# Kernel tuning notes

Measured on AMD Instinct MI355X. Metric: run time of the kernel, lower is better.

Reference implementation:

```python
import jax, jax.numpy as jnp
import numpy as np

B, IN, OUT = 512, 1023, 512
CLIP = 2.0
LN_EPS = 1e-5


def setup_inputs() -> dict:
    key = jax.random.key(0)
    ks = jax.random.split(key, 10)
    x = jax.random.normal(ks[0], (B, IN), dtype=jnp.float32)
    hebb = jax.random.normal(ks[1], (B, IN + 1, OUT), dtype=jnp.float32)
    weight = 0.001 * jax.random.normal(ks[2], (IN + 1, OUT), dtype=jnp.float32)
    alpha = 0.001 * jax.random.normal(ks[3], (IN + 1, OUT), dtype=jnp.float32)
    ln_gamma = jnp.ones((OUT,), dtype=jnp.float32)
    ln_beta = jnp.zeros((OUT,), dtype=jnp.float32)
    # modulator: Linear(OUT, 1)
    mod_w = jax.random.uniform(ks[4], (1, OUT), dtype=jnp.float32,
                               minval=-1.0, maxval=1.0) / np.sqrt(OUT)
    mod_b = jax.random.uniform(ks[5], (1,), dtype=jnp.float32,
                               minval=-1.0, maxval=1.0) / np.sqrt(OUT)
    # modfanout: Linear(1, OUT)
    fan_w = jax.random.uniform(ks[6], (OUT, 1), dtype=jnp.float32,
                               minval=-1.0, maxval=1.0)
    fan_b = jax.random.uniform(ks[7], (OUT,), dtype=jnp.float32,
                               minval=-1.0, maxval=1.0)
    return {"x": x, "hebb": hebb, "weight": weight, "alpha": alpha,
            "ln_gamma": ln_gamma, "ln_beta": ln_beta,
            "mod_w": mod_w, "mod_b": mod_b, "fan_w": fan_w, "fan_b": fan_b}


def reference(x, hebb, weight, alpha, ln_gamma, ln_beta, mod_w, mod_b, fan_w, fan_b):
    # pad bias column of ones: [B, IN+1]
    xp = jnp.concatenate([x, jnp.ones((x.shape[0], 1), dtype=x.dtype)], axis=-1)
    # per-sample effective weights: [B, IN+1, OUT]
    w_eff = weight[None] + alpha[None] * hebb
    y_pre = jnp.einsum('bi,bio->bo', xp, w_eff)  # [B, OUT]
    # LayerNorm over last dim
    mu = jnp.mean(y_pre, axis=-1, keepdims=True)
    var = jnp.mean(jnp.square(y_pre - mu), axis=-1, keepdims=True)
    y = jnp.tanh(ln_gamma * (y_pre - mu) * jax.lax.rsqrt(var + LN_EPS) + ln_beta)
    # modulator scalar per sample: [B, 1]
    m = jnp.tanh(y @ mod_w.T + mod_b)
    # fanout eta: [B, 1, OUT]
    eta = m[:, :, None] * fan_w[:, 0][None, None, :] + fan_b[None, None, :]
    # outer-product Hebbian update: [B, IN+1, OUT]
    delta = eta * (xp[:, :, None] * y[:, None, :])
    hebb_new = jnp.clip(hebb + delta, -CLIP, CLIP)
    return (y, m, hebb_new)
```

## Files before the change

### kernel.cpp

```cpp
#include <hip/hip_runtime.h>
#include <cstddef>

#define B_       512
#define IN_      1023
#define INP1     1024
#define OUT_     512
#define OUT4     128
#define CLIPV    2.0f
#define LNEPS    1e-5f
#define SLABS    4
#define SLABROWS 256

typedef float fx4 __attribute__((ext_vector_type(4)));

__device__ __forceinline__ float2 block_reduce2(float a, float b, float2* lds) {
    #pragma unroll
    for (int off = 32; off; off >>= 1) {
        a += __shfl_down(a, off, 64);
        b += __shfl_down(b, off, 64);
    }
    const int lane = threadIdx.x & 63;
    const int wid  = threadIdx.x >> 6;
    const int nw   = blockDim.x >> 6;
    if (lane == 0) lds[wid] = make_float2(a, b);
    __syncthreads();
    if (wid == 0) {
        float2 v = (lane < nw) ? lds[lane] : make_float2(0.f, 0.f);
        a = v.x; b = v.y;
        #pragma unroll
        for (int off = 8; off; off >>= 1) {
            a += __shfl_down(a, off, 64);
            b += __shfl_down(b, off, 64);
        }
        if (lane == 0) lds[0] = make_float2(a, b);
    }
    __syncthreads();
    float2 r = lds[0];
    __syncthreads();
    return r;
}

__global__ __launch_bounds__(256) void k1a_partial(
    const float* __restrict__ x, const float* __restrict__ hebb,
    const float* __restrict__ weight, const float* __restrict__ alpha,
    float* __restrict__ ws_part)
{
    const int bs   = blockIdx.x;
    const int b    = bs >> 2;
    const int s    = bs & 3;
    const int tid  = threadIdx.x;
    const int o4   = tid & 127;
    const int half = tid >> 7;

    __shared__ float  xs[SLABROWS];
    __shared__ float4 part[2][OUT4];

    {
        const int i = s * SLABROWS + tid;
        xs[tid] = (i < IN_) ? x[(size_t)b * IN_ + i] : 1.0f;
    }
    __syncthreads();

    const int i0 = s * SLABROWS + half * 128;
    const float4* __restrict__ h4 = (const float4*)hebb  + ((size_t)b * INP1 + i0) * OUT4 + o4;
    const float4* __restrict__ w4 = (const float4*)weight + (size_t)i0 * OUT4 + o4;
    const float4* __restrict__ a4 = (const float4*)alpha  + (size_t)i0 * OUT4 + o4;
    const float* __restrict__ xk = xs + half * 128;

    float4 acc = make_float4(0.f, 0.f, 0.f, 0.f);
    #pragma unroll 4
    for (int k = 0; k < 128; ++k) {
        const float  xv = xk[k];
        const float4 h  = h4[(size_t)k * OUT4];
        const float4 w  = w4[(size_t)k * OUT4];
        const float4 a  = a4[(size_t)k * OUT4];
        acc.x = fmaf(xv, fmaf(a.x, h.x, w.x), acc.x);
        acc.y = fmaf(xv, fmaf(a.y, h.y, w.y), acc.y);
        acc.z = fmaf(xv, fmaf(a.z, h.z, w.z), acc.z);
        acc.w = fmaf(xv, fmaf(a.w, h.w, w.w), acc.w);
    }

    part[half][o4] = acc;
    __syncthreads();
    if (half == 0) {
        float4 p = part[0][o4];
        const float4 q = part[1][o4];
        p.x += q.x; p.y += q.y; p.z += q.z; p.w += q.w;
        ((float4*)ws_part)[(size_t)bs * OUT4 + o4] = p;
    }
}

__global__ __launch_bounds__(512) void k1b_ln_mod(
    const float* __restrict__ ws_part,
    const float* __restrict__ ln_g, const float* __restrict__ ln_b,
    const float* __restrict__ mod_w, const float* __restrict__ mod_b,
    float* __restrict__ y_out, float* __restrict__ m_out)
{
    const int b = blockIdx.x;
    const int o = threadIdx.x;
    __shared__ float2 rbuf[16];

    float ypre = 0.f;
    #pragma unroll
    for (int s = 0; s < SLABS; ++s)
        ypre += ws_part[((size_t)b * SLABS + s) * OUT_ + o];

    float2 ss = block_reduce2(ypre, ypre * ypre, rbuf);
    const float mu   = ss.x * (1.0f / OUT_);
    const float var  = ss.y * (1.0f / OUT_) - mu * mu;
    const float rstd = rsqrtf(var + LNEPS);

    const float yv = tanhf(fmaf(ln_g[o], (ypre - mu) * rstd, ln_b[o]));
    y_out[(size_t)b * OUT_ + o] = yv;

    float2 ms = block_reduce2(yv * mod_w[o], 0.f, rbuf);
    if (o == 0) m_out[b] = tanhf(ms.x + mod_b[0]);
}

__global__ __launch_bounds__(256) void k2_update(
    const float* __restrict__ x, const float* __restrict__ hebb,
    const float* __restrict__ y, const float* __restrict__ m,
    const float* __restrict__ fan_w, const float* __restrict__ fan_b,
    float* __restrict__ hebb_out)
{
    const int bsr  = (int)gridDim.x - 1 - (int)blockIdx.x;
    const int b    = bsr >> 2;
    const int s    = bsr & 3;
    const int tid  = threadIdx.x;
    const int o4   = tid & 127;
    const int half = tid >> 7;

    __shared__ float xs[SLABROWS];
    {
        const int i = s * SLABROWS + tid;
        xs[tid] = (i < IN_) ? x[(size_t)b * IN_ + i] : 1.0f;
    }
    __syncthreads();

    const float  mb = m[b];
    const float4 yv = ((const float4*)y)[(size_t)b * OUT4 + o4];
    const float4 fw = ((const float4*)fan_w)[o4];
    const float4 fb = ((const float4*)fan_b)[o4];
    float4 coef;
    coef.x = fmaf(mb, fw.x, fb.x) * yv.x;
    coef.y = fmaf(mb, fw.y, fb.y) * yv.y;
    coef.z = fmaf(mb, fw.z, fb.z) * yv.z;
    coef.w = fmaf(mb, fw.w, fb.w) * yv.w;

    const int i0 = s * SLABROWS + half * 128;
    const size_t base = ((size_t)b * INP1 + i0) * OUT4 + o4;
    const fx4* __restrict__ h4  = (const fx4*)hebb + base;
    fx4* __restrict__       ho4 = (fx4*)hebb_out + base;
    const float* __restrict__ xk = xs + half * 128;

    #pragma unroll 4
    for (int k = 0; k < 128; ++k) {
        const float xv = xk[k];
        const fx4   h  = h4[(size_t)k * OUT4];
        fx4 r;
        r.x = fminf(fmaxf(fmaf(coef.x, xv, h.x), -CLIPV), CLIPV);
        r.y = fminf(fmaxf(fmaf(coef.y, xv, h.y), -CLIPV), CLIPV);
        r.z = fminf(fmaxf(fmaf(coef.z, xv, h.z), -CLIPV), CLIPV);
        r.w = fminf(fmaxf(fmaf(coef.w, xv, h.w), -CLIPV), CLIPV);
        __builtin_nontemporal_store(r, &ho4[(size_t)k * OUT4]);
    }
}

extern "C" void kernel_launch(void* const* d_in, const int* in_sizes, int n_in,
                              void* d_out, int out_size, void* d_ws, size_t ws_size,
                              hipStream_t stream) {
    const float* x      = (const float*)d_in[0];
    const float* hebb   = (const float*)d_in[1];
    const float* weight = (const float*)d_in[2];
    const float* alpha  = (const float*)d_in[3];
    const float* ln_g   = (const float*)d_in[4];
    const float* ln_b   = (const float*)d_in[5];
    const float* mod_w  = (const float*)d_in[6];
    const float* mod_b  = (const float*)d_in[7];
    const float* fan_w  = (const float*)d_in[8];
    const float* fan_b  = (const float*)d_in[9];

    float* out      = (float*)d_out;
    float* y_out    = out;
    float* m_out    = out + (size_t)B_ * OUT_;
    float* hebb_out = m_out + B_;

    const size_t part_bytes = (size_t)B_ * SLABS * OUT_ * sizeof(float);
    float* ws_part = (ws_size >= part_bytes) ? (float*)d_ws
                                             : hebb_out;

    k1a_partial<<<B_ * SLABS, 256, 0, stream>>>(x, hebb, weight, alpha, ws_part);
    k1b_ln_mod<<<B_, OUT_, 0, stream>>>(ws_part, ln_g, ln_b, mod_w, mod_b,
                                        y_out, m_out);
    k2_update<<<B_ * SLABS, 256, 0, stream>>>(x, hebb, y_out, m_out,
                                              fan_w, fan_b, hebb_out);
}
```

Measured before the change: 648.8 us.

## Batch samples so hebb reread hits cache and fuse LayerNorm into update kernel

Processes the batch in chunks of 64 samples, running the partial matvec and then a fused LayerNorm/modulator/Hebbian-update kernel per chunk. A chunk's hebb slice is small enough that the update kernel's second read may be served from the last-level cache rather than HBM. The LayerNorm kernel is folded into the update kernel, with each row-slab block recomputing it redundantly. The cost is more kernel launches, per-chunk tail effects, and dropping the workspace-size fallback.

```diff
diff --git a/kernel.cpp b/kernel.cpp
--- a/kernel.cpp
+++ b/kernel.cpp
@@ -1,15 +1,20 @@
 #include <hip/hip_runtime.h>
 #include <cstddef>
 
-#define B_       512
-#define IN_      1023
-#define INP1     1024
-#define OUT_     512
-#define OUT4     128
-#define CLIPV    2.0f
-#define LNEPS    1e-5f
-#define SLABS    4
-#define SLABROWS 256
+#define B_     512
+#define IN_    1023
+#define INP1   1024
+#define OUT_   512
+#define OUT4   128
+#define CLIPV  2.0f
+#define LNEPS  1e-5f
+
+#define BATCH  64
+#define NBATCH 8
+#define S1     16
+#define R1     64
+#define S2     8
+#define R2     128
 
 typedef float fx4 __attribute__((ext_vector_type(4)));
 
@@ -43,33 +48,34 @@
 __global__ __launch_bounds__(256) void k1a_partial(
     const float* __restrict__ x, const float* __restrict__ hebb,
     const float* __restrict__ weight, const float* __restrict__ alpha,
-    float* __restrict__ ws_part)
+    float* __restrict__ ws_part, int b0)
 {
-    const int bs   = blockIdx.x;
-    const int b    = bs >> 2;
-    const int s    = bs & 3;
-    const int tid  = threadIdx.x;
+    const int blk  = (int)blockIdx.x;
+    const int bl   = blk >> 4;
+    const int s    = blk & (S1 - 1);
+    const int b    = b0 + bl;
+    const int tid  = (int)threadIdx.x;
     const int o4   = tid & 127;
     const int half = tid >> 7;
 
-    __shared__ float  xs[SLABROWS];
+    __shared__ float  xs[R1];
     __shared__ float4 part[2][OUT4];
 
-    {
-        const int i = s * SLABROWS + tid;
-        xs[tid] = (i < IN_) ? x[(size_t)b * IN_ + i] : 1.0f;
-    }
-    __syncthreads();
-
-    const int i0 = s * SLABROWS + half * 128;
-    const float4* __restrict__ h4 = (const float4*)hebb  + ((size_t)b * INP1 + i0) * OUT4 + o4;
-    const float4* __restrict__ w4 = (const float4*)weight + (size_t)i0 * OUT4 + o4;
-    const float4* __restrict__ a4 = (const float4*)alpha  + (size_t)i0 * OUT4 + o4;
-    const float* __restrict__ xk = xs + half * 128;
+    if (tid < R1) {
+        const int row = s * R1 + tid;
+        xs[tid] = (row < IN_) ? x[(size_t)b * IN_ + row] : 1.0f;
+    }
+    __syncthreads();
+
+    const int r0 = s * R1 + half * 32;
+    const float4* __restrict__ h4 = (const float4*)hebb   + ((size_t)b * INP1 + r0) * OUT4 + o4;
+    const float4* __restrict__ w4 = (const float4*)weight + (size_t)r0 * OUT4 + o4;
+    const float4* __restrict__ a4 = (const float4*)alpha  + (size_t)r0 * OUT4 + o4;
+    const float*  __restrict__ xk = xs + half * 32;
 
     float4 acc = make_float4(0.f, 0.f, 0.f, 0.f);
-    #pragma unroll 4
-    for (int k = 0; k < 128; ++k) {
+    #pragma unroll 8
+    for (int k = 0; k < 32; ++k) {
         const float  xv = xk[k];
         const float4 h  = h4[(size_t)k * OUT4];
         const float4 w  = w4[(size_t)k * OUT4];
@@ -86,75 +92,72 @@
         float4 p = part[0][o4];
         const float4 q = part[1][o4];
         p.x += q.x; p.y += q.y; p.z += q.z; p.w += q.w;
-        ((float4*)ws_part)[(size_t)bs * OUT4 + o4] = p;
-    }
-}
-
-__global__ __launch_bounds__(512) void k1b_ln_mod(
+        ((float4*)ws_part)[((size_t)bl * S1 + s) * OUT4 + o4] = p;
+    }
+}
+
+__global__ __launch_bounds__(512) void k2f_ln_update(
+    const float* __restrict__ x, const float* __restrict__ hebb,
     const float* __restrict__ ws_part,
     const float* __restrict__ ln_g, const float* __restrict__ ln_b,
     const float* __restrict__ mod_w, const float* __restrict__ mod_b,
-    float* __restrict__ y_out, float* __restrict__ m_out)
+    const float* __restrict__ fan_w, const float* __restrict__ fan_b,
+    float* __restrict__ y_out, float* __restrict__ m_out,
+    float* __restrict__ hebb_out, int b0)
 {
-    const int b = blockIdx.x;
-    const int o = threadIdx.x;
+    const int blk = (int)blockIdx.x;
+    const int bl  = blk >> 3;
+    const int s   = blk & (S2 - 1);
+    const int b   = b0 + bl;
+    const int tid = (int)threadIdx.x;
+    const int o   = tid;
+
+    __shared__ float  xs[R2];
+    __shared__ float  y_lds[OUT_];
     __shared__ float2 rbuf[16];
 
     float ypre = 0.f;
     #pragma unroll
-    for (int s = 0; s < SLABS; ++s)
-        ypre += ws_part[((size_t)b * SLABS + s) * OUT_ + o];
+    for (int t = 0; t < S1; ++t)
+        ypre += ws_part[((size_t)bl * S1 + t) * OUT_ + o];
 
     float2 ss = block_reduce2(ypre, ypre * ypre, rbuf);
     const float mu   = ss.x * (1.0f / OUT_);
     const float var  = ss.y * (1.0f / OUT_) - mu * mu;
     const float rstd = rsqrtf(var + LNEPS);
-
-    const float yv = tanhf(fmaf(ln_g[o], (ypre - mu) * rstd, ln_b[o]));
-    y_out[(size_t)b * OUT_ + o] = yv;
+    const float yv   = tanhf(fmaf(ln_g[o], (ypre - mu) * rstd, ln_b[o]));
+    y_lds[o] = yv;
+    if (s == 0) y_out[(size_t)b * OUT_ + o] = yv;
 
     float2 ms = block_reduce2(yv * mod_w[o], 0.f, rbuf);
-    if (o == 0) m_out[b] = tanhf(ms.x + mod_b[0]);
-}
-
-__global__ __launch_bounds__(256) void k2_update(
-    const float* __restrict__ x, const float* __restrict__ hebb,
-    const float* __restrict__ y, const float* __restrict__ m,
-    const float* __restrict__ fan_w, const float* __restrict__ fan_b,
-    float* __restrict__ hebb_out)
-{
-    const int bsr  = (int)gridDim.x - 1 - (int)blockIdx.x;
-    const int b    = bsr >> 2;
-    const int s    = bsr & 3;
-    const int tid  = threadIdx.x;
-    const int o4   = tid & 127;
-    const int half = tid >> 7;
-
-    __shared__ float xs[SLABROWS];
-    {
-        const int i = s * SLABROWS + tid;
-        xs[tid] = (i < IN_) ? x[(size_t)b * IN_ + i] : 1.0f;
-    }
-    __syncthreads();
-
-    const float  mb = m[b];
-    const float4 yv = ((const float4*)y)[(size_t)b * OUT4 + o4];
-    const float4 fw = ((const float4*)fan_w)[o4];
-    const float4 fb = ((const float4*)fan_b)[o4];
-    float4 coef;
-    coef.x = fmaf(mb, fw.x, fb.x) * yv.x;
-    coef.y = fmaf(mb, fw.y, fb.y) * yv.y;
-    coef.z = fmaf(mb, fw.z, fb.z) * yv.z;
-    coef.w = fmaf(mb, fw.w, fb.w) * yv.w;
-
-    const int i0 = s * SLABROWS + half * 128;
-    const size_t base = ((size_t)b * INP1 + i0) * OUT4 + o4;
+    const float mval = tanhf(ms.x + mod_b[0]);
+    if (s == 0 && tid == 0) m_out[b] = mval;
+
+    if (tid < R2) {
+        const int row = s * R2 + tid;
+        xs[tid] = (row < IN_) ? x[(size_t)b * IN_ + row] : 1.0f;
+    }
+    __syncthreads();
+
+    const int o4 = tid & 127;
+    const int q  = tid >> 7;
+    const float4 yv4 = ((const float4*)y_lds)[o4];
+    const float4 fw  = ((const float4*)fan_w)[o4];
+    const float4 fb  = ((const float4*)fan_b)[o4];
+    fx4 coef;
+    coef.x = fmaf(mval, fw.x, fb.x) * yv4.x;
+    coef.y = fmaf(mval, fw.y, fb.y) * yv4.y;
+    coef.z = fmaf(mval, fw.z, fb.z) * yv4.z;
+    coef.w = fmaf(mval, fw.w, fb.w) * yv4.w;
+
+    const int r0 = s * R2 + q * 32;
+    const size_t base = ((size_t)b * INP1 + r0) * OUT4 + o4;
     const fx4* __restrict__ h4  = (const fx4*)hebb + base;
     fx4* __restrict__       ho4 = (fx4*)hebb_out + base;
-    const float* __restrict__ xk = xs + half * 128;
-
-    #pragma unroll 4
-    for (int k = 0; k < 128; ++k) {
+    const float* __restrict__ xk = xs + q * 32;
+
+    #pragma unroll 8
+    for (int k = 0; k < 32; ++k) {
         const float xv = xk[k];
         const fx4   h  = h4[(size_t)k * OUT4];
         fx4 r;
@@ -185,13 +188,15 @@
     float* m_out    = out + (size_t)B_ * OUT_;
     float* hebb_out = m_out + B_;
 
-    const size_t part_bytes = (size_t)B_ * SLABS * OUT_ * sizeof(float);
-    float* ws_part = (ws_size >= part_bytes) ? (float*)d_ws
-                                             : hebb_out;
-
-    k1a_partial<<<B_ * SLABS, 256, 0, stream>>>(x, hebb, weight, alpha, ws_part);
-    k1b_ln_mod<<<B_, OUT_, 0, stream>>>(ws_part, ln_g, ln_b, mod_w, mod_b,
-                                        y_out, m_out);
-    k2_update<<<B_ * SLABS, 256, 0, stream>>>(x, hebb, y_out, m_out,
-                                              fan_w, fan_b, hebb_out);
-}
+    float* ws_part = (float*)d_ws;
+
+    for (int batch = 0; batch < NBATCH; ++batch) {
+        const int b0 = batch * BATCH;
+        k1a_partial<<<BATCH * S1, 256, 0, stream>>>(x, hebb, weight, alpha,
+                                                    ws_part, b0);
+        k2f_ln_update<<<BATCH * S2, 512, 0, stream>>>(x, hebb, ws_part,
+                                                      ln_g, ln_b, mod_w, mod_b,
+                                                      fan_w, fan_b,
+                                                      y_out, m_out, hebb_out, b0);
+    }
+}
```

Result: slower. 673.9 us (+3.9%).

## Fuse all stages into one kernel with per-sample spin sync and register-held hebb

Applied to the files above, without the earlier changes.

Replaces the three-kernel pipeline with one kernel launched with 16 strip blocks per sample. Each block loads its 64 rows of hebb into registers, computes partial matvecs and signals a per-sample counter. Strip 0 spins on that counter, computes LayerNorm and the modulator, then sets a flag that the other strips spin on before applying the clipped update from the registers they already hold. This is meant to drop the second full read of hebb and two kernel launches. In exchange it adds a memset, spin-wait latency, and deadlock risk if the blocks that must finish first are not resident at the same time as the blocks waiting on them.

```diff
diff --git a/kernel.cpp b/kernel.cpp
--- a/kernel.cpp
+++ b/kernel.cpp
@@ -1,15 +1,18 @@
 #include <hip/hip_runtime.h>
 #include <cstddef>
 
-#define B_       512
-#define IN_      1023
-#define INP1     1024
-#define OUT_     512
-#define OUT4     128
-#define CLIPV    2.0f
-#define LNEPS    1e-5f
-#define SLABS    4
-#define SLABROWS 256
+#define B_     512
+#define IN_    1023
+#define INP1   1024
+#define OUT_   512
+#define OUT4   128
+#define CLIPV  2.0f
+#define LNEPS  1e-5f
+
+#define STRIPS 16
+#define ROWS   64
+#define FT     512
+#define KPT    16
 
 typedef float fx4 __attribute__((ext_vector_type(4)));
 
@@ -40,15 +43,143 @@
     return r;
 }
 
+__global__ __launch_bounds__(FT, 2) void fused_spin(
+    const float* __restrict__ x, const float* __restrict__ hebb,
+    const float* __restrict__ weight, const float* __restrict__ alpha,
+    const float* __restrict__ ln_g, const float* __restrict__ ln_b,
+    const float* __restrict__ mod_w, const float* __restrict__ mod_b,
+    const float* __restrict__ fan_w, const float* __restrict__ fan_b,
+    float* __restrict__ y_out, float* __restrict__ m_out,
+    float* __restrict__ hebb_out,
+    float* __restrict__ ws_part, int* __restrict__ cnt, int* __restrict__ flag)
+{
+    const int blk = (int)blockIdx.x;
+    const int b   = blk >> 4;
+    const int s   = blk & (STRIPS - 1);
+    const int tid = (int)threadIdx.x;
+    const int o4  = tid & 127;
+    const int rg  = tid >> 7;
+
+    __shared__ float  xs[ROWS];
+    __shared__ float4 part[4][OUT4];
+    __shared__ float  y_lds[OUT_];
+    __shared__ float2 rbuf[16];
+
+    const int row0 = s * ROWS;
+    if (tid < ROWS) {
+        const int row = row0 + tid;
+        xs[tid] = (row < IN_) ? x[(size_t)b * IN_ + row] : 1.0f;
+    }
+    __syncthreads();
+
+    const fx4*    __restrict__ h4 = (const fx4*)hebb    + ((size_t)b * INP1 + row0 + rg) * OUT4 + o4;
+    const float4* __restrict__ w4 = (const float4*)weight + (size_t)(row0 + rg) * OUT4 + o4;
+    const float4* __restrict__ a4 = (const float4*)alpha  + (size_t)(row0 + rg) * OUT4 + o4;
+
+    fx4 h[KPT];
+    float4 acc = make_float4(0.f, 0.f, 0.f, 0.f);
+    #pragma unroll
+    for (int k = 0; k < KPT; ++k) {
+        h[k] = __builtin_nontemporal_load(&h4[(size_t)k * (4 * OUT4)]);
+        const float4 wv = w4[(size_t)k * (4 * OUT4)];
+        const float4 av = a4[(size_t)k * (4 * OUT4)];
+        const float  xv = xs[rg + 4 * k];
+        acc.x = fmaf(xv, fmaf(av.x, h[k].x, wv.x), acc.x);
+        acc.y = fmaf(xv, fmaf(av.y, h[k].y, wv.y), acc.y);
+        acc.z = fmaf(xv, fmaf(av.z, h[k].z, wv.z), acc.z);
+        acc.w = fmaf(xv, fmaf(av.w, h[k].w, wv.w), acc.w);
+    }
+
+    part[rg][o4] = acc;
+    __syncthreads();
+    if (rg == 0) {
+        float4 p = part[0][o4];
+        const float4 q1 = part[1][o4], q2 = part[2][o4], q3 = part[3][o4];
+        p.x += q1.x + q2.x + q3.x;
+        p.y += q1.y + q2.y + q3.y;
+        p.z += q1.z + q2.z + q3.z;
+        p.w += q1.w + q2.w + q3.w;
+        ((float4*)ws_part)[((size_t)b * STRIPS + s) * OUT4 + o4] = p;
+    }
+    __syncthreads();
+    if (tid == 0)
+        __hip_atomic_fetch_add(&cnt[b], 1, __ATOMIC_RELEASE, __HIP_MEMORY_SCOPE_AGENT);
+
+    float mval;
+    if (s == 0) {
+        if (tid == 0) {
+            while (__hip_atomic_load(&cnt[b], __ATOMIC_ACQUIRE, __HIP_MEMORY_SCOPE_AGENT) < STRIPS)
+                __builtin_amdgcn_s_sleep(2);
+        }
+        __syncthreads();
+
+        const int o = tid;
+        float ypre = 0.f;
+        #pragma unroll
+        for (int t = 0; t < STRIPS; ++t)
+            ypre += ws_part[((size_t)b * STRIPS + t) * OUT_ + o];
+
+        float2 ss = block_reduce2(ypre, ypre * ypre, rbuf);
+        const float mu   = ss.x * (1.0f / OUT_);
+        const float var  = ss.y * (1.0f / OUT_) - mu * mu;
+        const float rstd = rsqrtf(var + LNEPS);
+        const float yv   = tanhf(fmaf(ln_g[o], (ypre - mu) * rstd, ln_b[o]));
+        y_lds[o] = yv;
+        y_out[(size_t)b * OUT_ + o] = yv;
+
+        float2 ms = block_reduce2(yv * mod_w[o], 0.f, rbuf);
+        mval = tanhf(ms.x + mod_b[0]);
+        if (tid == 0) m_out[b] = mval;
+
+        __syncthreads();
+        if (tid == 0)
+            __hip_atomic_store(&flag[b], 1, __ATOMIC_RELEASE, __HIP_MEMORY_SCOPE_AGENT);
+    } else {
+        if (tid == 0) {
+            while (__hip_atomic_load(&flag[b], __ATOMIC_ACQUIRE, __HIP_MEMORY_SCOPE_AGENT) == 0)
+                __builtin_amdgcn_s_sleep(2);
+        }
+        __syncthreads();
+        y_lds[tid] = y_out[(size_t)b * OUT_ + tid];
+        mval = m_out[b];
+        __syncthreads();
+    }
+
+    const float4 yv4 = ((const float4*)y_lds)[o4];
+    const float4 fw  = ((const float4*)fan_w)[o4];
+    const float4 fb  = ((const float4*)fan_b)[o4];
+    fx4 coef;
+    coef.x = fmaf(mval, fw.x, fb.x) * yv4.x;
+    coef.y = fmaf(mval, fw.y, fb.y) * yv4.y;
+    coef.z = fmaf(mval, fw.z, fb.z) * yv4.z;
+    coef.w = fmaf(mval, fw.w, fb.w) * yv4.w;
+
+    fx4* __restrict__ ho4 = (fx4*)hebb_out + ((size_t)b * INP1 + row0 + rg) * OUT4 + o4;
+    #pragma unroll
+    for (int k = 0; k < KPT; ++k) {
+        const float xv = xs[rg + 4 * k];
+        fx4 rr;
+        rr.x = fminf(fmaxf(fmaf(coef.x, xv, h[k].x), -CLIPV), CLIPV);
+        rr.y = fminf(fmaxf(fmaf(coef.y, xv, h[k].y), -CLIPV), CLIPV);
+        rr.z = fminf(fmaxf(fmaf(coef.z, xv, h[k].z), -CLIPV), CLIPV);
+        rr.w = fminf(fmaxf(fmaf(coef.w, xv, h[k].w), -CLIPV), CLIPV);
+        __builtin_nontemporal_store(rr, &ho4[(size_t)k * (4 * OUT4)]);
+    }
+}
+
+#define SLABS    4
+#define SLABROWS 256
+#define NBS      (B_ * SLABS)
+
 __global__ __launch_bounds__(256) void k1a_partial(
     const float* __restrict__ x, const float* __restrict__ hebb,
     const float* __restrict__ weight, const float* __restrict__ alpha,
     float* __restrict__ ws_part)
 {
-    const int bs   = blockIdx.x;
+    const int bs   = (int)blockIdx.x;
     const int b    = bs >> 2;
     const int s    = bs & 3;
-    const int tid  = threadIdx.x;
+    const int tid  = (int)threadIdx.x;
     const int o4   = tid & 127;
     const int half = tid >> 7;
 
@@ -96,8 +227,8 @@
     const float* __restrict__ mod_w, const float* __restrict__ mod_b,
     float* __restrict__ y_out, float* __restrict__ m_out)
 {
-    const int b = blockIdx.x;
-    const int o = threadIdx.x;
+    const int b = (int)blockIdx.x;
+    const int o = (int)threadIdx.x;
     __shared__ float2 rbuf[16];
 
     float ypre = 0.f;
@@ -123,10 +254,10 @@
     const float* __restrict__ fan_w, const float* __restrict__ fan_b,
     float* __restrict__ hebb_out)
 {
-    const int bsr  = (int)gridDim.x - 1 - (int)blockIdx.x;
+    const int bsr  = NBS - 1 - (int)blockIdx.x;
     const int b    = bsr >> 2;
     const int s    = bsr & 3;
-    const int tid  = threadIdx.x;
+    const int tid  = (int)threadIdx.x;
     const int o4   = tid & 127;
     const int half = tid >> 7;
 
@@ -185,13 +316,24 @@
     float* m_out    = out + (size_t)B_ * OUT_;
     float* hebb_out = m_out + B_;
 
-    const size_t part_bytes = (size_t)B_ * SLABS * OUT_ * sizeof(float);
-    float* ws_part = (ws_size >= part_bytes) ? (float*)d_ws
-                                             : hebb_out;
-
-    k1a_partial<<<B_ * SLABS, 256, 0, stream>>>(x, hebb, weight, alpha, ws_part);
-    k1b_ln_mod<<<B_, OUT_, 0, stream>>>(ws_part, ln_g, ln_b, mod_w, mod_b,
-                                        y_out, m_out);
-    k2_update<<<B_ * SLABS, 256, 0, stream>>>(x, hebb, y_out, m_out,
-                                              fan_w, fan_b, hebb_out);
-}
+    const size_t part_floats = (size_t)B_ * STRIPS * OUT_;
+    const size_t need = part_floats * sizeof(float) + 2 * B_ * sizeof(int);
+
+    if (ws_size >= need) {
+        float* ws_part = (float*)d_ws;
+        int*   cnt     = (int*)((char*)d_ws + part_floats * sizeof(float));
+        int*   flag    = cnt + B_;
+        hipMemsetAsync(cnt, 0, 2 * B_ * sizeof(int), stream);
+        fused_spin<<<B_ * STRIPS, FT, 0, stream>>>(
+            x, hebb, weight, alpha, ln_g, ln_b, mod_w, mod_b, fan_w, fan_b,
+            y_out, m_out, hebb_out, ws_part, cnt, flag);
+    } else {
+        const size_t part_bytes = (size_t)B_ * SLABS * OUT_ * sizeof(float);
+        float* ws_part = (ws_size >= part_bytes) ? (float*)d_ws : hebb_out;
+        k1a_partial<<<NBS, 256, 0, stream>>>(x, hebb, weight, alpha, ws_part);
+        k1b_ln_mod<<<B_, OUT_, 0, stream>>>(ws_part, ln_g, ln_b, mod_w, mod_b,
+                                            y_out, m_out);
+        k2_update<<<NBS, 256, 0, stream>>>(x, hebb, y_out, m_out,
+                                           fan_w, fan_b, hebb_out);
+    }
+}
```

Result: slower. 1.313 ms (+102.4%).

## Group 16 samples per block in first pass to reuse weight and alpha rows

Applied to the files above, without the earlier changes.

The first reduction kernel now gives each block 16 samples and a 64-row strip, so every loaded weight/alpha row is reused across 16 batch samples instead of being reloaded per sample. This cuts repeated weight and alpha reads, which were about two thirds of the loads in that pass. In exchange it uses 16 float4 accumulators per thread, serialises 16 LDS reduction rounds with barriers, and writes 16 partials per sample instead of 4, which makes the LayerNorm kernel read more. The dominant hebb traffic is unchanged.

```diff
diff --git a/kernel.cpp b/kernel.cpp
--- a/kernel.cpp
+++ b/kernel.cpp
@@ -1,15 +1,22 @@
 #include <hip/hip_runtime.h>
 #include <cstddef>
 
-#define B_       512
-#define IN_      1023
-#define INP1     1024
-#define OUT_     512
-#define OUT4     128
-#define CLIPV    2.0f
-#define LNEPS    1e-5f
-#define SLABS    4
-#define SLABROWS 256
+#define B_     512
+#define IN_    1023
+#define INP1   1024
+#define OUT_   512
+#define OUT4   128
+#define CLIPV  2.0f
+#define LNEPS  1e-5f
+
+#define G_      16
+#define NGRP    32
+#define RSTRIP  64
+#define NSID    16
+
+#define K2S     4
+#define K2ROWS  256
+#define NBS2    (B_ * K2S)
 
 typedef float fx4 __attribute__((ext_vector_type(4)));
 
@@ -40,53 +47,64 @@
     return r;
 }
 
-__global__ __launch_bounds__(256) void k1a_partial(
+__global__ __launch_bounds__(512, 4) void k1a_grouped(
     const float* __restrict__ x, const float* __restrict__ hebb,
     const float* __restrict__ weight, const float* __restrict__ alpha,
     float* __restrict__ ws_part)
 {
-    const int bs   = blockIdx.x;
-    const int b    = bs >> 2;
-    const int s    = bs & 3;
-    const int tid  = threadIdx.x;
-    const int o4   = tid & 127;
-    const int half = tid >> 7;
-
-    __shared__ float  xs[SLABROWS];
-    __shared__ float4 part[2][OUT4];
+    const int blk = (int)blockIdx.x;
+    const int gid = blk >> 4;
+    const int sid = blk & (NSID - 1);
+    const int b0  = gid * G_;
+    const int r0  = sid * RSTRIP;
+    const int tid = (int)threadIdx.x;
+    const int o4  = tid & 127;
+    const int rg  = tid >> 7;
+
+    __shared__ float  xs[G_][RSTRIP];
+    __shared__ float4 pl[4][OUT4];
 
     {
-        const int i = s * SLABROWS + tid;
-        xs[tid] = (i < IN_) ? x[(size_t)b * IN_ + i] : 1.0f;
-    }
-    __syncthreads();
-
-    const int i0 = s * SLABROWS + half * 128;
-    const float4* __restrict__ h4 = (const float4*)hebb  + ((size_t)b * INP1 + i0) * OUT4 + o4;
-    const float4* __restrict__ w4 = (const float4*)weight + (size_t)i0 * OUT4 + o4;
-    const float4* __restrict__ a4 = (const float4*)alpha  + (size_t)i0 * OUT4 + o4;
-    const float* __restrict__ xk = xs + half * 128;
-
-    float4 acc = make_float4(0.f, 0.f, 0.f, 0.f);
-    #pragma unroll 4
-    for (int k = 0; k < 128; ++k) {
-        const float  xv = xk[k];
-        const float4 h  = h4[(size_t)k * OUT4];
-        const float4 w  = w4[(size_t)k * OUT4];
-        const float4 a  = a4[(size_t)k * OUT4];
-        acc.x = fmaf(xv, fmaf(a.x, h.x, w.x), acc.x);
-        acc.y = fmaf(xv, fmaf(a.y, h.y, w.y), acc.y);
-        acc.z = fmaf(xv, fmaf(a.z, h.z, w.z), acc.z);
-        acc.w = fmaf(xv, fmaf(a.w, h.w, w.w), acc.w);
-    }
-
-    part[half][o4] = acc;
-    __syncthreads();
-    if (half == 0) {
-        float4 p = part[0][o4];
-        const float4 q = part[1][o4];
-        p.x += q.x; p.y += q.y; p.z += q.z; p.w += q.w;
-        ((float4*)ws_part)[(size_t)bs * OUT4 + o4] = p;
+        const int g = tid >> 5, j = tid & 31;
+        const int ra = r0 + j, rb = r0 + j + 32;
+        xs[g][j]      = (ra < IN_) ? x[(size_t)(b0 + g) * IN_ + ra] : 1.0f;
+        xs[g][j + 32] = (rb < IN_) ? x[(size_t)(b0 + g) * IN_ + rb] : 1.0f;
+    }
+    __syncthreads();
+
+    fx4 acc[G_];
+    #pragma unroll
+    for (int g = 0; g < G_; ++g) acc[g] = (fx4){0.f, 0.f, 0.f, 0.f};
+
+    for (int il = 0; il < 16; ++il) {
+        const int rr  = rg * 16 + il;
+        const int row = r0 + rr;
+        const float4 wv = ((const float4*)weight)[(size_t)row * OUT4 + o4];
+        const float4 av = ((const float4*)alpha )[(size_t)row * OUT4 + o4];
+        #pragma unroll
+        for (int g = 0; g < G_; ++g) {
+            const fx4 h = ((const fx4*)hebb)[((size_t)(b0 + g) * INP1 + row) * OUT4 + o4];
+            const float xv = xs[g][rr];
+            acc[g].x = fmaf(xv, fmaf(av.x, h.x, wv.x), acc[g].x);
+            acc[g].y = fmaf(xv, fmaf(av.y, h.y, wv.y), acc[g].y);
+            acc[g].z = fmaf(xv, fmaf(av.z, h.z, wv.z), acc[g].z);
+            acc[g].w = fmaf(xv, fmaf(av.w, h.w, wv.w), acc[g].w);
+        }
+    }
+
+    for (int g = 0; g < G_; ++g) {
+        pl[rg][o4] = make_float4(acc[g].x, acc[g].y, acc[g].z, acc[g].w);
+        __syncthreads();
+        if (rg == 0) {
+            float4 p = pl[0][o4];
+            const float4 q1 = pl[1][o4], q2 = pl[2][o4], q3 = pl[3][o4];
+            p.x += q1.x + q2.x + q3.x;
+            p.y += q1.y + q2.y + q3.y;
+            p.z += q1.z + q2.z + q3.z;
+            p.w += q1.w + q2.w + q3.w;
+            ((float4*)ws_part)[((size_t)(b0 + g) * NSID + sid) * OUT4 + o4] = p;
+        }
+        __syncthreads();
     }
 }
 
@@ -96,14 +114,14 @@
     const float* __restrict__ mod_w, const float* __restrict__ mod_b,
     float* __restrict__ y_out, float* __restrict__ m_out)
 {
-    const int b = blockIdx.x;
-    const int o = threadIdx.x;
+    const int b = (int)blockIdx.x;
+    const int o = (int)threadIdx.x;
     __shared__ float2 rbuf[16];
 
     float ypre = 0.f;
     #pragma unroll
-    for (int s = 0; s < SLABS; ++s)
-        ypre += ws_part[((size_t)b * SLABS + s) * OUT_ + o];
+    for (int s = 0; s < NSID; ++s)
+        ypre += ws_part[((size_t)b * NSID + s) * OUT_ + o];
 
     float2 ss = block_reduce2(ypre, ypre * ypre, rbuf);
     const float mu   = ss.x * (1.0f / OUT_);
@@ -123,16 +141,16 @@
     const float* __restrict__ fan_w, const float* __restrict__ fan_b,
     float* __restrict__ hebb_out)
 {
-    const int bsr  = (int)gridDim.x - 1 - (int)blockIdx.x;
+    const int bsr  = NBS2 - 1 - (int)blockIdx.x;
     const int b    = bsr >> 2;
     const int s    = bsr & 3;
-    const int tid  = threadIdx.x;
+    const int tid  = (int)threadIdx.x;
     const int o4   = tid & 127;
     const int half = tid >> 7;
 
-    __shared__ float xs[SLABROWS];
+    __shared__ float xs[K2ROWS];
     {
-        const int i = s * SLABROWS + tid;
+        const int i = s * K2ROWS + tid;
         xs[tid] = (i < IN_) ? x[(size_t)b * IN_ + i] : 1.0f;
     }
     __syncthreads();
@@ -147,7 +165,7 @@
     coef.z = fmaf(mb, fw.z, fb.z) * yv.z;
     coef.w = fmaf(mb, fw.w, fb.w) * yv.w;
 
-    const int i0 = s * SLABROWS + half * 128;
+    const int i0 = s * K2ROWS + half * 128;
     const size_t base = ((size_t)b * INP1 + i0) * OUT4 + o4;
     const fx4* __restrict__ h4  = (const fx4*)hebb + base;
     fx4* __restrict__       ho4 = (fx4*)hebb_out + base;
@@ -185,13 +203,14 @@
     float* m_out    = out + (size_t)B_ * OUT_;
     float* hebb_out = m_out + B_;
 
-    const size_t part_bytes = (size_t)B_ * SLABS * OUT_ * sizeof(float);
-    float* ws_part = (ws_size >= part_bytes) ? (float*)d_ws
-                                             : hebb_out;
-
-    k1a_partial<<<B_ * SLABS, 256, 0, stream>>>(x, hebb, weight, alpha, ws_part);
+    const size_t part_bytes = (size_t)B_ * NSID * OUT_ * sizeof(float);
+    float* ws_part = (ws_size >= part_bytes)
+                   ? (float*)d_ws
+                   : hebb_out;
+
+    k1a_grouped<<<NGRP * NSID, 512, 0, stream>>>(x, hebb, weight, alpha, ws_part);
     k1b_ln_mod<<<B_, OUT_, 0, stream>>>(ws_part, ln_g, ln_b, mod_w, mod_b,
                                         y_out, m_out);
-    k2_update<<<B_ * SLABS, 256, 0, stream>>>(x, hebb, y_out, m_out,
-                                              fan_w, fan_b, hebb_out);
-}
+    k2_update<<<NBS2, 256, 0, stream>>>(x, hebb, y_out, m_out,
+                                        fan_w, fan_b, hebb_out);
+}
```

Result: slower. 703.3 us (+8.4%).
